# Kernel tuning notes

Hardware: AMD Instinct MI355X
Metric: run time of the kernel (lower is better)

Reference implementation:

```python
import jax, jax.numpy as jnp
import numpy as np

LN_EPS = 1e-5

def _conv2d(x, w, b, pad):
    # x: [B,C,H,W], w: [O,I,kh,kw] -> [B,O,H,W]
    y = jax.lax.conv_general_dilated(
        x, w, window_strides=(1, 1), padding=[(pad, pad), (pad, pad)],
        dimension_numbers=('NCHW', 'OIHW', 'NCHW'))
    return y + b[None, :, None, None]

def setup_inputs() -> dict:
    key = jax.random.key(0)
    ks = jax.random.split(key, 12)
    B, C, H, W = 4, 256, 64, 64
    D = 64  # inner_projection
    s_in = 1.0 / np.sqrt(C)
    s_d1 = 1.0 / np.sqrt(D)
    s_d3 = 1.0 / np.sqrt(D * 9)
    return {
        'x':     jax.random.normal(ks[0], (B, C, H, W), jnp.float32),
        'w_in':  jax.random.normal(ks[1], (D, C, 1, 1), jnp.float32) * s_in,
        'b_in':  jnp.zeros((D,), jnp.float32),
        'wq':    jax.random.normal(ks[2], (D, D, 3, 3), jnp.float32) * s_d3,
        'bq':    jnp.zeros((D,), jnp.float32),
        'wk':    jax.random.normal(ks[3], (D, D, 3, 3), jnp.float32) * s_d3,
        'bk':    jnp.zeros((D,), jnp.float32),
        'wv':    jax.random.normal(ks[4], (D, D, 3, 3), jnp.float32) * s_d3,
        'bv':    jnp.zeros((D,), jnp.float32),
        'w_out': jax.random.normal(ks[5], (C, D, 1, 1), jnp.float32) * s_d1,
        'b_out': jnp.zeros((C,), jnp.float32),
        'gamma': jax.random.normal(ks[6], (1,), jnp.float32) * 0.1,
        'ln_w':  jnp.ones((C,), jnp.float32),
        'ln_b':  jnp.zeros((C,), jnp.float32),
    }

def _attention(q, k, v):
    # full-pixel attention, NO 1/sqrt(d) scale (matches source)
    B, C, H, W = v.shape
    N = H * W
    qf = q.reshape(B, -1, N)   # [B,d,N]
    kf = k.reshape(B, -1, N)
    vf = v.reshape(B, -1, N)
    energy = jnp.einsum('bci,bcj->bij', qf, kf)      # [B,N,N] = Q^T K
    attn = jax.nn.softmax(energy, axis=-1)
    out = jnp.einsum('bcj,bij->bci', vf, attn)        # V @ attn^T
    return out.reshape(B, C, H, W)

def _layernorm2d(x, w, b):
    # normalize over channel dim per pixel (LayerNorm2d)
    mu = jnp.mean(x, axis=1, keepdims=True)
    var = jnp.var(x, axis=1, keepdims=True)
    xn = (x - mu) * jax.lax.rsqrt(var + LN_EPS)
    return xn * w[None, :, None, None] + b[None, :, None, None]

def reference(x, w_in, b_in, wq, bq, wk, bk, wv, bv, w_out, b_out, gamma, ln_w, ln_b):
    att = _conv2d(x, w_in, b_in, 0)          # inner projection [B,D,H,W]
    q = _conv2d(att, wq, bq, 1)
    k = _conv2d(att, wk, bk, 1)
    v = _conv2d(att, wv, bv, 1)
    att = _attention(q, k, v)
    att = _conv2d(att, w_out, b_out, 0)       # outer projection [B,C,H,W]
    return _layernorm2d(gamma * x + att, ln_w, ln_b)
```

## Files before the change

kernel.cpp:

```cpp
#include <hip/hip_runtime.h>
#include <hip/hip_bf16.h>

#define BB 4
#define CC 256
#define DD 64
#define HH 64
#define WW 64
#define NN 4096
#define NSPLIT 8
#define SM_SHIFT2 92.332482616893664f
#define LOG2E 1.4426950408889634f

typedef __hip_bfloat16 bf16;
typedef __attribute__((ext_vector_type(8))) short bf16x8;
typedef __attribute__((ext_vector_type(4))) float f32x4;
typedef __attribute__((ext_vector_type(4))) short s16x4;

#define MFMA16(a, b, c) __builtin_amdgcn_mfma_f32_16x16x32_bf16(a, b, c, 0, 0, 0)

#if __has_builtin(__builtin_amdgcn_mfma_f32_16x16x16bf16_1k)
static __device__ __forceinline__ f32x4 MFMA16K(s16x4 a, s16x4 b, f32x4 c) {
  return __builtin_amdgcn_mfma_f32_16x16x16bf16_1k(a, b, c, 0, 0, 0);
}
#else
static __device__ __forceinline__ f32x4 MFMA16K(s16x4 a, s16x4 b, f32x4 c) {
  f32x4 d;
  asm("v_mfma_f32_16x16x16_bf16 %0, %1, %2, %3"
      : "=&v"(d) : "v"(a), "v"(b), "v"(c));
  return d;
}
#endif

#if __has_builtin(__builtin_amdgcn_exp2f)
#define EXP2F(x) __builtin_amdgcn_exp2f(x)
#else
#define EXP2F(x) exp2f(x)
#endif

static __device__ __forceinline__ float ldin(const void* p, size_t i, bool isb) {
  return isb ? __bfloat162float(((const bf16*)p)[i]) : ((const float*)p)[i];
}
static __device__ __forceinline__ void stout(void* p, size_t i, float v, bool isb) {
  if (isb) ((bf16*)p)[i] = __float2bfloat16(v);
  else     ((float*)p)[i] = v;
}
static __device__ __forceinline__ unsigned pack2(bf16 a, bf16 b) {
  unsigned short ua = *reinterpret_cast<unsigned short*>(&a);
  unsigned short ub = *reinterpret_cast<unsigned short*>(&b);
  return (unsigned)ua | ((unsigned)ub << 16);
}
static __device__ __forceinline__ bool probe_bf16(const unsigned* lnw) {
  return lnw[0] == 0x3F803F80u;
}

__global__ __launch_bounds__(256) void k_wt(
    const void* __restrict__ wq, const void* __restrict__ wk,
    const void* __restrict__ wv, const void* __restrict__ w_in,
    const void* __restrict__ w_out,
    bf16* __restrict__ Wth, bf16* __restrict__ Wtl,
    bf16* __restrict__ Win_h, bf16* __restrict__ Win_l,
    bf16* __restrict__ Wo_h, bf16* __restrict__ Wo_l,
    const unsigned* __restrict__ lnw) {
  const bool isb = probe_bf16(lnw);
  int u = blockIdx.x * 256 + threadIdx.x;
  if (u < 110592) {
    int c3 = u / 36864, rem = u % 36864;
    int tap = rem / 4096, r2 = rem % 4096;
    int oc = r2 >> 6, ic = r2 & 63;
    const void* w = (c3 == 0) ? wq : ((c3 == 1) ? wk : wv);
    float v = ldin(w, (size_t)oc * 576 + ic * 9 + tap, isb);
    bf16 h = __float2bfloat16(v);
    Wth[u] = h;
    Wtl[u] = __float2bfloat16(v - __bfloat162float(h));
  } else if (u < 126976) {
    int v2 = u - 110592;
    float v = ldin(w_in, v2, isb);
    bf16 h = __float2bfloat16(v);
    Win_h[v2] = h;
    Win_l[v2] = __float2bfloat16(v - __bfloat162float(h));
  } else {
    int v2 = u - 126976;
    float v = ldin(w_out, v2, isb);
    bf16 h = __float2bfloat16(v);
    Wo_h[v2] = h;
    Wo_l[v2] = __float2bfloat16(v - __bfloat162float(h));
  }
}

__global__ __launch_bounds__(256) void k_conv_in(
    const void* __restrict__ x,
    const bf16* __restrict__ Win_h, const bf16* __restrict__ Win_l,
    const void* __restrict__ bias, bf16* __restrict__ att_h,
    bf16* __restrict__ att_l, const unsigned* __restrict__ lnw) {
  __shared__ __align__(16) short Xh[32 * 64];
  __shared__ __align__(16) short Xl[32 * 64];
  const bool isb = probe_bf16(lnw);
  const int b = blockIdx.y, n0 = blockIdx.x * 32;
  const int t = threadIdx.x;
  const int w = t >> 6, lane = t & 63, quad = lane >> 4, l16 = lane & 15;
  const int l7 = l16 & 7;
  const size_t xoff = (size_t)b * CC * NN;
  f32x4 acc[2];
  #pragma unroll
  for (int nt = 0; nt < 2; ++nt)
    #pragma unroll
    for (int r = 0; r < 4; ++r)
      acc[nt][r] = ldin(bias, w * 16 + quad * 4 + r, isb);
  for (int c0 = 0; c0 < CC; c0 += 64) {
    __syncthreads();
    #pragma unroll
    for (int i = 0; i < 4; ++i) {
      int u = t + i * 256;
      int dd = u >> 5, n = u & 31;
      float v0 = ldin(x, xoff + (size_t)(c0 + 2 * dd) * NN + n0 + n, isb);
      float v1 = ldin(x, xoff + (size_t)(c0 + 2 * dd + 1) * NN + n0 + n, isb);
      bf16 h0 = __float2bfloat16(v0), h1 = __float2bfloat16(v1);
      bf16 l0 = __float2bfloat16(v0 - __bfloat162float(h0));
      bf16 l1 = __float2bfloat16(v1 - __bfloat162float(h1));
      int cs = ((dd >> 2) ^ (n & 7)) * 8 + ((2 * dd) & 7);
      *(unsigned*)&Xh[n * 64 + cs] = pack2(h0, h1);
      *(unsigned*)&Xl[n * 64 + cs] = pack2(l0, l1);
    }
    __syncthreads();
    #pragma unroll
    for (int kc = 0; kc < 2; ++kc) {
      size_t woff = (size_t)(w * 16 + l16) * 256 + c0 + kc * 32 + quad * 8;
      bf16x8 wh = *(const bf16x8*)(Win_h + woff);
      bf16x8 wl = *(const bf16x8*)(Win_l + woff);
      const int xo = ((kc * 4 + quad) ^ l7) * 8;
      #pragma unroll
      for (int nt = 0; nt < 2; ++nt) {
        int rn = nt * 16 + l16;
        bf16x8 xh = *(const bf16x8*)&Xh[rn * 64 + xo];
        bf16x8 xl = *(const bf16x8*)&Xl[rn * 64 + xo];
        acc[nt] = MFMA16(wh, xh, acc[nt]);
        acc[nt] = MFMA16(wh, xl, acc[nt]);
        acc[nt] = MFMA16(wl, xh, acc[nt]);
      }
    }
  }
  #pragma unroll
  for (int nt = 0; nt < 2; ++nt) {
    size_t off = ((size_t)b * NN + n0 + nt * 16 + l16) * DD + w * 16 + quad * 4;
    bf16 h[4], l[4];
    #pragma unroll
    for (int r = 0; r < 4; ++r) {
      float v = acc[nt][r];
      h[r] = __float2bfloat16(v);
      l[r] = __float2bfloat16(v - __bfloat162float(h[r]));
    }
    *(uint2*)&att_h[off] = make_uint2(pack2(h[0], h[1]), pack2(h[2], h[3]));
    *(uint2*)&att_l[off] = make_uint2(pack2(l[0], l[1]), pack2(l[2], l[3]));
  }
}

__global__ __launch_bounds__(256) void k_conv3(
    const bf16* __restrict__ att_h, const bf16* __restrict__ att_l,
    const bf16* __restrict__ Wth, const bf16* __restrict__ Wtl,
    const void* __restrict__ bq, const void* __restrict__ bk,
    const void* __restrict__ bv,
    bf16* __restrict__ qth, bf16* __restrict__ qtl,
    bf16* __restrict__ kth, bf16* __restrict__ ktl,
    bf16* __restrict__ vt, const unsigned* __restrict__ lnw) {
  __shared__ __align__(16) short Ah[3 * 66 * 64];
  __shared__ __align__(16) short Al[3 * 66 * 64];
  float* o_s = reinterpret_cast<float*>(Ah);
  const bool isb = probe_bf16(lnw);
  const int y = blockIdx.x, b = blockIdx.y, c3 = blockIdx.z;
  const int t = threadIdx.x;
  const int w = t >> 6, lane = t & 63, quad = lane >> 4, l16 = lane & 15;
  const uint4 z4 = make_uint4(0, 0, 0, 0);
  #pragma unroll
  for (int r = 0; r < 3; ++r) {
    int yp = y + r - 1;
    bool ok = (unsigned)yp < 64u;
    const uint4* sh = (const uint4*)(att_h + ((size_t)b * NN + (size_t)yp * 64) * DD);
    const uint4* sl = (const uint4*)(att_l + ((size_t)b * NN + (size_t)yp * 64) * DD);
    #pragma unroll
    for (int ii = 0; ii < 2; ++ii) {
      int u = t + ii * 256;
      int xx = u >> 3, ch = u & 7;
      int rr = r * 66 + xx + 1;
      uint4 vh = ok ? sh[u] : z4;
      uint4 vl = ok ? sl[u] : z4;
      int cs = (ch ^ (rr & 7)) * 8;
      *(uint4*)&Ah[rr * 64 + cs] = vh;
      *(uint4*)&Al[rr * 64 + cs] = vl;
    }
    if (t < 16) {
      int rr = r * 66 + ((t & 1) ? 65 : 0);
      int cs = (t >> 1) * 8;
      *(uint4*)&Ah[rr * 64 + cs] = z4;
      *(uint4*)&Al[rr * 64 + cs] = z4;
    }
  }
  __syncthreads();
  const void* bp = (c3 == 0) ? bq : ((c3 == 1) ? bk : bv);
  const bf16* wth = Wth + (size_t)c3 * 9 * 4096;
  const bf16* wtl = Wtl + (size_t)c3 * 9 * 4096;
  f32x4 acc[4];
  #pragma unroll
  for (int nt = 0; nt < 4; ++nt)
    #pragma unroll
    for (int r = 0; r < 4; ++r)
      acc[nt][r] = ldin(bp, w * 16 + quad * 4 + r, isb);
  #pragma unroll
  for (int tap = 0; tap < 9; ++tap) {
    const int dy = tap / 3, dx = tap % 3;
    const int woff = tap * 4096 + (w * 16 + l16) * 64 + quad * 8;
    bf16x8 wh0 = *(const bf16x8*)(wth + woff);
    bf16x8 wh1 = *(const bf16x8*)(wth + woff + 32);
    bf16x8 wl0 = *(const bf16x8*)(wtl + woff);
    bf16x8 wl1 = *(const bf16x8*)(wtl + woff + 32);
    #pragma unroll
    for (int nt = 0; nt < 4; ++nt) {
      int rr = dy * 66 + nt * 16 + l16 + dx;
      int chA = (quad ^ (rr & 7)) * 8;
      int chB = ((quad + 4) ^ (rr & 7)) * 8;
      bf16x8 ah0 = *(const bf16x8*)&Ah[rr * 64 + chA];
      bf16x8 ah1 = *(const bf16x8*)&Ah[rr * 64 + chB];
      bf16x8 al0 = *(const bf16x8*)&Al[rr * 64 + chA];
      bf16x8 al1 = *(const bf16x8*)&Al[rr * 64 + chB];
      acc[nt] = MFMA16(wh0, ah0, acc[nt]);
      acc[nt] = MFMA16(wh1, ah1, acc[nt]);
      acc[nt] = MFMA16(wh0, al0, acc[nt]);
      acc[nt] = MFMA16(wh1, al1, acc[nt]);
      acc[nt] = MFMA16(wl0, ah0, acc[nt]);
      acc[nt] = MFMA16(wl1, ah1, acc[nt]);
    }
  }
  if (c3 < 2) {
    bf16* dh = (c3 == 0) ? qth : kth;
    bf16* dl = (c3 == 0) ? qtl : ktl;
    const float qsc = (c3 == 0) ? LOG2E : 1.0f;
    const size_t rowb = (size_t)b * NN + (size_t)y * 64;
    #pragma unroll
    for (int nt = 0; nt < 4; ++nt) {
      size_t off = (rowb + nt * 16 + l16) * DD + w * 16 + quad * 4;
      bf16 h[4], l[4];
      #pragma unroll
      for (int r = 0; r < 4; ++r) {
        float v = acc[nt][r] * qsc;
        h[r] = __float2bfloat16(v);
        l[r] = __float2bfloat16(v - __bfloat162float(h[r]));
      }
      *(uint2*)&dh[off] = make_uint2(pack2(h[0], h[1]), pack2(h[2], h[3]));
      *(uint2*)&dl[off] = make_uint2(pack2(l[0], l[1]), pack2(l[2], l[3]));
    }
  } else {
    __syncthreads();
    #pragma unroll
    for (int nt = 0; nt < 4; ++nt)
      #pragma unroll
      for (int r = 0; r < 4; ++r)
        o_s[(nt * 16 + l16) * 65 + w * 16 + quad * 4 + r] = acc[nt][r];
    __syncthreads();
    #pragma unroll
    for (int i = 0; i < 8; ++i) {
      int u = t + i * 256;
      int c = u >> 5, np = (u & 31) * 2;
      float v0 = o_s[np * 65 + c], v1 = o_s[(np + 1) * 65 + c];
      *(unsigned*)&vt[((size_t)b * DD + c) * NN + (size_t)y * 64 + np] =
          pack2(__float2bfloat16(v0), __float2bfloat16(v1));
    }
  }
}

__global__ __launch_bounds__(256) void k_attn(
    const bf16* __restrict__ qth, const bf16* __restrict__ qtl,
    const bf16* __restrict__ kth, const bf16* __restrict__ ktl,
    const bf16* __restrict__ vt, float* __restrict__ po,
    float* __restrict__ pl) {
  __shared__ __align__(16) short Kh[64 * 64];
  __shared__ __align__(16) short Kl[64 * 64];
  __shared__ __align__(16) short Vs[64 * 64];
  const int b = blockIdx.y, i0 = blockIdx.x * 128, sp = blockIdx.z;
  const int jt0 = sp * (64 / NSPLIT), jt1 = jt0 + (64 / NSPLIT);
  const int t = threadIdx.x;
  const int w = t >> 6, lane = t & 63, quad = lane >> 4, l16 = lane & 15;
  const int l7 = l16 & 7;
  const int xA = (quad ^ l7) * 8;
  const int xB = ((quad + 4) ^ l7) * 8;
  const int sr = t >> 2, m4 = t & 3, sg = m4 * 16;
  const int sc0 = ((2 * m4) ^ (sr & 7)) * 8;
  const int sc1 = ((2 * m4 + 1) ^ (sr & 7)) * 8;
  bf16x8 qf_h0[2], qf_h1[2], qf_l0[2], qf_l1[2];
  #pragma unroll
  for (int is = 0; is < 2; ++is) {
    size_t qoff = ((size_t)b * NN + i0 + is * 64 + w * 16 + l16) * DD + quad * 8;
    qf_h0[is] = *(const bf16x8*)(qth + qoff);
    qf_h1[is] = *(const bf16x8*)(qth + qoff + 32);
    qf_l0[is] = *(const bf16x8*)(qtl + qoff);
    qf_l1[is] = *(const bf16x8*)(qtl + qoff + 32);
  }
  uint4 kh0, kh1, kl0, kl1, vx0, vx1;
  {
    size_t koff = ((size_t)b * NN + jt0 * 64 + sr) * DD + sg;
    kh0 = ((const uint4*)(kth + koff))[0]; kh1 = ((const uint4*)(kth + koff))[1];
    kl0 = ((const uint4*)(ktl + koff))[0]; kl1 = ((const uint4*)(ktl + koff))[1];
    size_t voff = ((size_t)b * DD + sr) * NN + jt0 * 64 + sg;
    vx0 = ((const uint4*)(vt + voff))[0];  vx1 = ((const uint4*)(vt + voff))[1];
  }
  float l_run[2] = {0.f, 0.f};
  f32x4 oacc[4][2] = {};
  for (int jt = jt0; jt < jt1; ++jt) {
    __syncthreads();
    *(uint4*)&Kh[sr * 64 + sc0] = kh0;    *(uint4*)&Kh[sr * 64 + sc1] = kh1;
    *(uint4*)&Kl[sr * 64 + sc0] = kl0;    *(uint4*)&Kl[sr * 64 + sc1] = kl1;
    *(uint4*)&Vs[sr * 64 + sc0] = vx0;    *(uint4*)&Vs[sr * 64 + sc1] = vx1;
    __syncthreads();
    if (jt < jt1 - 1) {
      int j0n = (jt + 1) * 64;
      size_t koff = ((size_t)b * NN + j0n + sr) * DD + sg;
      kh0 = ((const uint4*)(kth + koff))[0]; kh1 = ((const uint4*)(kth + koff))[1];
      kl0 = ((const uint4*)(ktl + koff))[0]; kl1 = ((const uint4*)(ktl + koff))[1];
      size_t voff = ((size_t)b * DD + sr) * NN + j0n + sg;
      vx0 = ((const uint4*)(vt + voff))[0];  vx1 = ((const uint4*)(vt + voff))[1];
    }
    s16x4 pf[2][4];
    float psum[2] = {0.f, 0.f};
    #pragma unroll
    for (int mt = 0; mt < 4; ++mt) {
      int r0 = (mt * 16 + l16) * 64;
      bf16x8 kf_h0 = *(const bf16x8*)&Kh[r0 + xA];
      bf16x8 kf_h1 = *(const bf16x8*)&Kh[r0 + xB];
      bf16x8 kf_l0 = *(const bf16x8*)&Kl[r0 + xA];
      bf16x8 kf_l1 = *(const bf16x8*)&Kl[r0 + xB];
      #pragma unroll
      for (int is = 0; is < 2; ++is) {
        f32x4 c = {0.f, 0.f, 0.f, 0.f};
        c = MFMA16(kf_h0, qf_h0[is], c);
        c = MFMA16(kf_h1, qf_h1[is], c);
        c = MFMA16(kf_h0, qf_l0[is], c);
        c = MFMA16(kf_h1, qf_l1[is], c);
        c = MFMA16(kf_l0, qf_h0[is], c);
        c = MFMA16(kf_l1, qf_h1[is], c);
        s16x4 pk;
        float ps = 0.f;
        #pragma unroll
        for (int r = 0; r < 4; ++r) {
          float p = EXP2F(c[r] - SM_SHIFT2);
          bf16 ph = __float2bfloat16(p);
          ps += __bfloat162float(ph);
          pk[r] = *reinterpret_cast<short*>(&ph);
        }
        psum[is] += ps;
        pf[is][mt] = pk;
      }
    }
    #pragma unroll
    for (int is = 0; is < 2; ++is) {
      float ps = psum[is];
      ps += __shfl_xor(ps, 16, 64);
      ps += __shfl_xor(ps, 32, 64);
      l_run[is] += ps;
    }
    #pragma unroll
    for (int mt = 0; mt < 4; ++mt) {
      int rv = (mt * 16 + l16) * 64;
      #pragma unroll
      for (int kt = 0; kt < 4; ++kt) {
        s16x4 vf = *(const s16x4*)
            &Vs[rv + ((kt * 2 + (quad >> 1)) ^ l7) * 8 + (quad & 1) * 4];
        oacc[mt][0] = MFMA16K(vf, pf[0][kt], oacc[mt][0]);
        oacc[mt][1] = MFMA16K(vf, pf[1][kt], oacc[mt][1]);
      }
    }
  }
  const size_t SEGC = (size_t)BB * DD * NN;
  #pragma unroll
  for (int is = 0; is < 2; ++is) {
    const int ig = i0 + is * 64 + w * 16 + l16;
    #pragma unroll
    for (int mt = 0; mt < 4; ++mt)
      #pragma unroll
      for (int r = 0; r < 4; ++r) {
        int c = mt * 16 + quad * 4 + r;
        po[(size_t)sp * SEGC + ((size_t)b * DD + c) * NN + ig] = oacc[mt][is][r];
      }
    if (quad == 0) pl[((size_t)sp * BB + b) * NN + ig] = l_run[is];
  }
}

__global__ __launch_bounds__(256) void k_out_ln(
    const float* __restrict__ po, const float* __restrict__ pl,
    const void* __restrict__ x,
    const bf16* __restrict__ Wo_h, const bf16* __restrict__ Wo_l,
    const void* __restrict__ bias, const void* __restrict__ gamma,
    const void* __restrict__ lw, const void* __restrict__ lb,
    void* __restrict__ out, const unsigned* __restrict__ lnw) {
  __shared__ __align__(16) short Ahs[32 * 64];
  __shared__ __align__(16) short Als[32 * 64];
  __shared__ float inv_s[32];
  __shared__ float red1[32 * 4], red2[32 * 4];
  __shared__ float mu_s[32], rs_s[32];
  __shared__ float lw_s[256], lb_s[256];
  const bool isb = probe_bf16(lnw);
  const int b = blockIdx.y, n0 = blockIdx.x * 32;
  const int t = threadIdx.x;
  const int w = t >> 6, lane = t & 63, quad = lane >> 4, l16 = lane & 15;
  const int l7 = l16 & 7;
  const size_t SEGC = (size_t)BB * DD * NN;
  if (t < 32) {
    int i = n0 + t;
    float lsum = 0.f;
    #pragma unroll
    for (int s = 0; s < NSPLIT; ++s) lsum += pl[((size_t)s * BB + b) * NN + i];
    inv_s[t] = 1.f / lsum;
  }
  lw_s[t] = ldin(lw, t, isb);
  lb_s[t] = ldin(lb, t, isb);
  const float g = ldin(gamma, 0, isb);
  __syncthreads();
  #pragma unroll
  for (int i = 0; i < 4; ++i) {
    int u = t + i * 256;
    int dd = u >> 5, n = u & 31;
    size_t base = ((size_t)b * DD + 2 * dd) * NN + n0 + n;
    float v0 = 0.f, v1 = 0.f;
    #pragma unroll
    for (int s = 0; s < NSPLIT; ++s) {
      v0 += po[(size_t)s * SEGC + base];
      v1 += po[(size_t)s * SEGC + base + NN];
    }
    float inv = inv_s[n];
    v0 *= inv; v1 *= inv;
    bf16 h0 = __float2bfloat16(v0), h1 = __float2bfloat16(v1);
    bf16 l0 = __float2bfloat16(v0 - __bfloat162float(h0));
    bf16 l1 = __float2bfloat16(v1 - __bfloat162float(h1));
    int cs = ((dd >> 2) ^ (n & 7)) * 8 + ((2 * dd) & 7);
    *(unsigned*)&Ahs[n * 64 + cs] = pack2(h0, h1);
    *(unsigned*)&Als[n * 64 + cs] = pack2(l0, l1);
  }
  f32x4 acc[4][2];
  #pragma unroll
  for (int oct = 0; oct < 4; ++oct)
    #pragma unroll
    for (int r = 0; r < 4; ++r) {
      float bo = ldin(bias, w * 64 + oct * 16 + quad * 4 + r, isb);
      #pragma unroll
      for (int nt = 0; nt < 2; ++nt) acc[oct][nt][r] = bo;
    }
  __syncthreads();
  #pragma unroll
  for (int oct = 0; oct < 4; ++oct) {
    const int base = w * 64 + oct * 16;
    #pragma unroll
    for (int kc = 0; kc < 2; ++kc) {
      size_t woff = (size_t)(base + l16) * 64 + kc * 32 + quad * 8;
      bf16x8 wh = *(const bf16x8*)(Wo_h + woff);
      bf16x8 wl = *(const bf16x8*)(Wo_l + woff);
      const int xo = ((kc * 4 + quad) ^ l7) * 8;
      #pragma unroll
      for (int nt = 0; nt < 2; ++nt) {
        int rn = nt * 16 + l16;
        bf16x8 ah = *(const bf16x8*)&Ahs[rn * 64 + xo];
        bf16x8 al = *(const bf16x8*)&Als[rn * 64 + xo];
        acc[oct][nt] = MFMA16(wh, ah, acc[oct][nt]);
        acc[oct][nt] = MFMA16(wh, al, acc[oct][nt]);
        acc[oct][nt] = MFMA16(wl, ah, acc[oct][nt]);
      }
    }
  }
  #pragma unroll
  for (int nt = 0; nt < 2; ++nt) {
    int nn = nt * 16 + l16;
    float s1 = 0.f, s2 = 0.f;
    #pragma unroll
    for (int oct = 0; oct < 4; ++oct)
      #pragma unroll
      for (int r = 0; r < 4; ++r) {
        int oc = w * 64 + oct * 16 + quad * 4 + r;
        float xv = ldin(x, ((size_t)b * CC + oc) * NN + n0 + nn, isb);
        float y = acc[oct][nt][r] + g * xv;
        acc[oct][nt][r] = y;
        s1 += y; s2 += y * y;
      }
    s1 += __shfl_xor(s1, 16, 64); s1 += __shfl_xor(s1, 32, 64);
    s2 += __shfl_xor(s2, 16, 64); s2 += __shfl_xor(s2, 32, 64);
    if (quad == 0) { red1[nn * 4 + w] = s1; red2[nn * 4 + w] = s2; }
  }
  __syncthreads();
  if (t < 32) {
    float sm = red1[t * 4] + red1[t * 4 + 1] + red1[t * 4 + 2] + red1[t * 4 + 3];
    float sq = red2[t * 4] + red2[t * 4 + 1] + red2[t * 4 + 2] + red2[t * 4 + 3];
    float mu = sm * (1.f / 256.f);
    float var = sq * (1.f / 256.f) - mu * mu;
    mu_s[t] = mu;
    rs_s[t] = rsqrtf(var + 1e-5f);
  }
  __syncthreads();
  #pragma unroll
  for (int nt = 0; nt < 2; ++nt) {
    int nn = nt * 16 + l16;
    float mu = mu_s[nn], rs = rs_s[nn];
    #pragma unroll
    for (int oct = 0; oct < 4; ++oct)
      #pragma unroll
      for (int r = 0; r < 4; ++r) {
        int oc = w * 64 + oct * 16 + quad * 4 + r;
        float o = (acc[oct][nt][r] - mu) * rs * lw_s[oc] + lb_s[oc];
        stout(out, ((size_t)b * CC + oc) * NN + n0 + nn, o, isb);
      }
  }
}

extern "C" void kernel_launch(void* const* d_in, const int* in_sizes, int n_in,
                              void* d_out, int out_size, void* d_ws, size_t ws_size,
                              hipStream_t stream) {
  const void* x     = d_in[0];
  const void* w_in  = d_in[1];
  const void* b_in  = d_in[2];
  const void* wq    = d_in[3];
  const void* bq    = d_in[4];
  const void* wk    = d_in[5];
  const void* bk    = d_in[6];
  const void* wv    = d_in[7];
  const void* bv    = d_in[8];
  const void* w_out = d_in[9];
  const void* b_out = d_in[10];
  const void* gamma = d_in[11];
  const void* ln_w  = d_in[12];
  const void* ln_b  = d_in[13];

  const size_t SEG = (size_t)BB * DD * NN;
  char*  p     = (char*)d_ws;
  bf16*  att_h = (bf16*)p;  p += SEG * 2;
  bf16*  att_l = (bf16*)p;  p += SEG * 2;
  bf16*  qth   = (bf16*)p;  p += SEG * 2;
  bf16*  qtl   = (bf16*)p;  p += SEG * 2;
  bf16*  kth   = (bf16*)p;  p += SEG * 2;
  bf16*  ktl   = (bf16*)p;  p += SEG * 2;
  bf16*  vt    = (bf16*)p;  p += SEG * 2;
  float* po    = (float*)p; p += (size_t)NSPLIT * SEG * 4;
  float* pl    = (float*)p; p += (size_t)NSPLIT * BB * NN * 4;
  bf16*  Wth   = (bf16*)p;  p += 110592 * 2;
  bf16*  Wtl   = (bf16*)p;  p += 110592 * 2;
  bf16*  Win_h = (bf16*)p;  p += 16384 * 2;
  bf16*  Win_l = (bf16*)p;  p += 16384 * 2;
  bf16*  Wo_h  = (bf16*)p;  p += 16384 * 2;
  bf16*  Wo_l  = (bf16*)p;  p += 16384 * 2;
  const unsigned* lnw = (const unsigned*)ln_w;

  k_wt<<<560, 256, 0, stream>>>(wq, wk, wv, w_in, w_out, Wth, Wtl,
                                Win_h, Win_l, Wo_h, Wo_l, lnw);
  k_conv_in<<<dim3(NN / 32, BB), 256, 0, stream>>>(x, Win_h, Win_l, b_in,
                                                   att_h, att_l, lnw);
  k_conv3<<<dim3(64, BB, 3), 256, 0, stream>>>(att_h, att_l, Wth, Wtl,
                                               bq, bk, bv,
                                               qth, qtl, kth, ktl, vt, lnw);
  k_attn<<<dim3(NN / 128, BB, NSPLIT), 256, 0, stream>>>(qth, qtl, kth, ktl, vt,
                                                         po, pl);
  k_out_ln<<<dim3(NN / 32, BB), 256, 0, stream>>>(po, pl, x, Wo_h, Wo_l,
                                                  b_out, gamma, ln_w, ln_b,
                                                  d_out, lnw);
}
```

Measured before the change: 177.2 us.

## Double-buffer attention K/V tiles, halve split count, fuse conv3 q/k/v into one block

The attention kernel now double-buffers the K/V tiles in shared memory, cutting one barrier per iteration so the next tile's stores overlap compute. It also raises wave priority around the MFMA sections. The split count over keys drops from 8 to 4, which reduces partial-output traffic and reduction work in the output kernel but also halves the number of attention blocks. The 3x3 conv kernel now loops over q, k and v inside one block instead of launching three grid slices, so the staged input rows are reused, at the cost of fewer blocks running in parallel.

```diff
diff --git a/kernel.cpp b/kernel.cpp
--- a/kernel.cpp
+++ b/kernel.cpp
@@ -7,7 +7,7 @@
 #define HH 64
 #define WW 64
 #define NN 4096
-#define NSPLIT 8
+#define NSPLIT 4
 #define SM_SHIFT2 92.332482616893664f
 #define LOG2E 1.4426950408889634f
 
@@ -166,7 +166,7 @@
   __shared__ __align__(16) short Al[3 * 66 * 64];
   float* o_s = reinterpret_cast<float*>(Ah);
   const bool isb = probe_bf16(lnw);
-  const int y = blockIdx.x, b = blockIdx.y, c3 = blockIdx.z;
+  const int y = blockIdx.x, b = blockIdx.y;
   const int t = threadIdx.x;
   const int w = t >> 6, lane = t & 63, quad = lane >> 4, l16 = lane & 15;
   const uint4 z4 = make_uint4(0, 0, 0, 0);
@@ -195,73 +195,76 @@
     }
   }
   __syncthreads();
-  const void* bp = (c3 == 0) ? bq : ((c3 == 1) ? bk : bv);
-  const bf16* wth = Wth + (size_t)c3 * 9 * 4096;
-  const bf16* wtl = Wtl + (size_t)c3 * 9 * 4096;
-  f32x4 acc[4];
-  #pragma unroll
-  for (int nt = 0; nt < 4; ++nt)
-    #pragma unroll
-    for (int r = 0; r < 4; ++r)
-      acc[nt][r] = ldin(bp, w * 16 + quad * 4 + r, isb);
-  #pragma unroll
-  for (int tap = 0; tap < 9; ++tap) {
-    const int dy = tap / 3, dx = tap % 3;
-    const int woff = tap * 4096 + (w * 16 + l16) * 64 + quad * 8;
-    bf16x8 wh0 = *(const bf16x8*)(wth + woff);
-    bf16x8 wh1 = *(const bf16x8*)(wth + woff + 32);
-    bf16x8 wl0 = *(const bf16x8*)(wtl + woff);
-    bf16x8 wl1 = *(const bf16x8*)(wtl + woff + 32);
-    #pragma unroll
-    for (int nt = 0; nt < 4; ++nt) {
-      int rr = dy * 66 + nt * 16 + l16 + dx;
-      int chA = (quad ^ (rr & 7)) * 8;
-      int chB = ((quad + 4) ^ (rr & 7)) * 8;
-      bf16x8 ah0 = *(const bf16x8*)&Ah[rr * 64 + chA];
-      bf16x8 ah1 = *(const bf16x8*)&Ah[rr * 64 + chB];
-      bf16x8 al0 = *(const bf16x8*)&Al[rr * 64 + chA];
-      bf16x8 al1 = *(const bf16x8*)&Al[rr * 64 + chB];
-      acc[nt] = MFMA16(wh0, ah0, acc[nt]);
-      acc[nt] = MFMA16(wh1, ah1, acc[nt]);
-      acc[nt] = MFMA16(wh0, al0, acc[nt]);
-      acc[nt] = MFMA16(wh1, al1, acc[nt]);
-      acc[nt] = MFMA16(wl0, ah0, acc[nt]);
-      acc[nt] = MFMA16(wl1, ah1, acc[nt]);
-    }
-  }
-  if (c3 < 2) {
-    bf16* dh = (c3 == 0) ? qth : kth;
-    bf16* dl = (c3 == 0) ? qtl : ktl;
-    const float qsc = (c3 == 0) ? LOG2E : 1.0f;
-    const size_t rowb = (size_t)b * NN + (size_t)y * 64;
-    #pragma unroll
-    for (int nt = 0; nt < 4; ++nt) {
-      size_t off = (rowb + nt * 16 + l16) * DD + w * 16 + quad * 4;
-      bf16 h[4], l[4];
-      #pragma unroll
-      for (int r = 0; r < 4; ++r) {
-        float v = acc[nt][r] * qsc;
-        h[r] = __float2bfloat16(v);
-        l[r] = __float2bfloat16(v - __bfloat162float(h[r]));
-      }
-      *(uint2*)&dh[off] = make_uint2(pack2(h[0], h[1]), pack2(h[2], h[3]));
-      *(uint2*)&dl[off] = make_uint2(pack2(l[0], l[1]), pack2(l[2], l[3]));
-    }
-  } else {
-    __syncthreads();
+  #pragma unroll 1
+  for (int c3 = 0; c3 < 3; ++c3) {
+    const void* bp = (c3 == 0) ? bq : ((c3 == 1) ? bk : bv);
+    const bf16* wth = Wth + (size_t)c3 * 9 * 4096;
+    const bf16* wtl = Wtl + (size_t)c3 * 9 * 4096;
+    f32x4 acc[4];
     #pragma unroll
     for (int nt = 0; nt < 4; ++nt)
       #pragma unroll
       for (int r = 0; r < 4; ++r)
-        o_s[(nt * 16 + l16) * 65 + w * 16 + quad * 4 + r] = acc[nt][r];
-    __syncthreads();
-    #pragma unroll
-    for (int i = 0; i < 8; ++i) {
-      int u = t + i * 256;
-      int c = u >> 5, np = (u & 31) * 2;
-      float v0 = o_s[np * 65 + c], v1 = o_s[(np + 1) * 65 + c];
-      *(unsigned*)&vt[((size_t)b * DD + c) * NN + (size_t)y * 64 + np] =
-          pack2(__float2bfloat16(v0), __float2bfloat16(v1));
+        acc[nt][r] = ldin(bp, w * 16 + quad * 4 + r, isb);
+    #pragma unroll
+    for (int tap = 0; tap < 9; ++tap) {
+      const int dy = tap / 3, dx = tap % 3;
+      const int woff = tap * 4096 + (w * 16 + l16) * 64 + quad * 8;
+      bf16x8 wh0 = *(const bf16x8*)(wth + woff);
+      bf16x8 wh1 = *(const bf16x8*)(wth + woff + 32);
+      bf16x8 wl0 = *(const bf16x8*)(wtl + woff);
+      bf16x8 wl1 = *(const bf16x8*)(wtl + woff + 32);
+      #pragma unroll
+      for (int nt = 0; nt < 4; ++nt) {
+        int rr = dy * 66 + nt * 16 + l16 + dx;
+        int chA = (quad ^ (rr & 7)) * 8;
+        int chB = ((quad + 4) ^ (rr & 7)) * 8;
+        bf16x8 ah0 = *(const bf16x8*)&Ah[rr * 64 + chA];
+        bf16x8 ah1 = *(const bf16x8*)&Ah[rr * 64 + chB];
+        bf16x8 al0 = *(const bf16x8*)&Al[rr * 64 + chA];
+        bf16x8 al1 = *(const bf16x8*)&Al[rr * 64 + chB];
+        acc[nt] = MFMA16(wh0, ah0, acc[nt]);
+        acc[nt] = MFMA16(wh1, ah1, acc[nt]);
+        acc[nt] = MFMA16(wh0, al0, acc[nt]);
+        acc[nt] = MFMA16(wh1, al1, acc[nt]);
+        acc[nt] = MFMA16(wl0, ah0, acc[nt]);
+        acc[nt] = MFMA16(wl1, ah1, acc[nt]);
+      }
+    }
+    if (c3 < 2) {
+      bf16* dh = (c3 == 0) ? qth : kth;
+      bf16* dl = (c3 == 0) ? qtl : ktl;
+      const float qsc = (c3 == 0) ? LOG2E : 1.0f;
+      const size_t rowb = (size_t)b * NN + (size_t)y * 64;
+      #pragma unroll
+      for (int nt = 0; nt < 4; ++nt) {
+        size_t off = (rowb + nt * 16 + l16) * DD + w * 16 + quad * 4;
+        bf16 h[4], l[4];
+        #pragma unroll
+        for (int r = 0; r < 4; ++r) {
+          float v = acc[nt][r] * qsc;
+          h[r] = __float2bfloat16(v);
+          l[r] = __float2bfloat16(v - __bfloat162float(h[r]));
+        }
+        *(uint2*)&dh[off] = make_uint2(pack2(h[0], h[1]), pack2(h[2], h[3]));
+        *(uint2*)&dl[off] = make_uint2(pack2(l[0], l[1]), pack2(l[2], l[3]));
+      }
+    } else {
+      __syncthreads();
+      #pragma unroll
+      for (int nt = 0; nt < 4; ++nt)
+        #pragma unroll
+        for (int r = 0; r < 4; ++r)
+          o_s[(nt * 16 + l16) * 65 + w * 16 + quad * 4 + r] = acc[nt][r];
+      __syncthreads();
+      #pragma unroll
+      for (int i = 0; i < 8; ++i) {
+        int u = t + i * 256;
+        int c = u >> 5, np = (u & 31) * 2;
+        float v0 = o_s[np * 65 + c], v1 = o_s[(np + 1) * 65 + c];
+        *(unsigned*)&vt[((size_t)b * DD + c) * NN + (size_t)y * 64 + np] =
+            pack2(__float2bfloat16(v0), __float2bfloat16(v1));
+      }
     }
   }
 }
@@ -271,9 +274,9 @@
     const bf16* __restrict__ kth, const bf16* __restrict__ ktl,
     const bf16* __restrict__ vt, float* __restrict__ po,
     float* __restrict__ pl) {
-  __shared__ __align__(16) short Kh[64 * 64];
-  __shared__ __align__(16) short Kl[64 * 64];
-  __shared__ __align__(16) short Vs[64 * 64];
+  __shared__ __align__(16) short Kh[2][64 * 64];
+  __shared__ __align__(16) short Kl[2][64 * 64];
+  __shared__ __align__(16) short Vs[2][64 * 64];
   const int b = blockIdx.y, i0 = blockIdx.x * 128, sp = blockIdx.z;
   const int jt0 = sp * (64 / NSPLIT), jt1 = jt0 + (64 / NSPLIT);
   const int t = threadIdx.x;
@@ -301,14 +304,14 @@
     size_t voff = ((size_t)b * DD + sr) * NN + jt0 * 64 + sg;
     vx0 = ((const uint4*)(vt + voff))[0];  vx1 = ((const uint4*)(vt + voff))[1];
   }
+  *(uint4*)&Kh[0][sr * 64 + sc0] = kh0;  *(uint4*)&Kh[0][sr * 64 + sc1] = kh1;
+  *(uint4*)&Kl[0][sr * 64 + sc0] = kl0;  *(uint4*)&Kl[0][sr * 64 + sc1] = kl1;
+  *(uint4*)&Vs[0][sr * 64 + sc0] = vx0;  *(uint4*)&Vs[0][sr * 64 + sc1] = vx1;
+  __syncthreads();
   float l_run[2] = {0.f, 0.f};
   f32x4 oacc[4][2] = {};
+  int p = 0;
   for (int jt = jt0; jt < jt1; ++jt) {
-    __syncthreads();
-    *(uint4*)&Kh[sr * 64 + sc0] = kh0;    *(uint4*)&Kh[sr * 64 + sc1] = kh1;
-    *(uint4*)&Kl[sr * 64 + sc0] = kl0;    *(uint4*)&Kl[sr * 64 + sc1] = kl1;
-    *(uint4*)&Vs[sr * 64 + sc0] = vx0;    *(uint4*)&Vs[sr * 64 + sc1] = vx1;
-    __syncthreads();
     if (jt < jt1 - 1) {
       int j0n = (jt + 1) * 64;
       size_t koff = ((size_t)b * NN + j0n + sr) * DD + sg;
@@ -317,15 +320,19 @@
       size_t voff = ((size_t)b * DD + sr) * NN + j0n + sg;
       vx0 = ((const uint4*)(vt + voff))[0];  vx1 = ((const uint4*)(vt + voff))[1];
     }
+    const short* khp = Kh[p];
+    const short* klp = Kl[p];
+    const short* vsp = Vs[p];
     s16x4 pf[2][4];
     float psum[2] = {0.f, 0.f};
     #pragma unroll
     for (int mt = 0; mt < 4; ++mt) {
       int r0 = (mt * 16 + l16) * 64;
-      bf16x8 kf_h0 = *(const bf16x8*)&Kh[r0 + xA];
-      bf16x8 kf_h1 = *(const bf16x8*)&Kh[r0 + xB];
-      bf16x8 kf_l0 = *(const bf16x8*)&Kl[r0 + xA];
-      bf16x8 kf_l1 = *(const bf16x8*)&Kl[r0 + xB];
+      bf16x8 kf_h0 = *(const bf16x8*)&khp[r0 + xA];
+      bf16x8 kf_h1 = *(const bf16x8*)&khp[r0 + xB];
+      bf16x8 kf_l0 = *(const bf16x8*)&klp[r0 + xA];
+      bf16x8 kf_l1 = *(const bf16x8*)&klp[r0 + xB];
+      __builtin_amdgcn_s_setprio(1);
       #pragma unroll
       for (int is = 0; is < 2; ++is) {
         f32x4 c = {0.f, 0.f, 0.f, 0.f};
@@ -339,14 +346,15 @@
         float ps = 0.f;
         #pragma unroll
         for (int r = 0; r < 4; ++r) {
-          float p = EXP2F(c[r] - SM_SHIFT2);
-          bf16 ph = __float2bfloat16(p);
+          float pexp = EXP2F(c[r] - SM_SHIFT2);
+          bf16 ph = __float2bfloat16(pexp);
           ps += __bfloat162float(ph);
           pk[r] = *reinterpret_cast<short*>(&ph);
         }
         psum[is] += ps;
         pf[is][mt] = pk;
       }
+      __builtin_amdgcn_s_setprio(0);
     }
     #pragma unroll
     for (int is = 0; is < 2; ++is) {
@@ -355,17 +363,29 @@
       ps += __shfl_xor(ps, 32, 64);
       l_run[is] += ps;
     }
+    __builtin_amdgcn_s_setprio(1);
     #pragma unroll
     for (int mt = 0; mt < 4; ++mt) {
       int rv = (mt * 16 + l16) * 64;
       #pragma unroll
       for (int kt = 0; kt < 4; ++kt) {
         s16x4 vf = *(const s16x4*)
-            &Vs[rv + ((kt * 2 + (quad >> 1)) ^ l7) * 8 + (quad & 1) * 4];
+            &vsp[rv + ((kt * 2 + (quad >> 1)) ^ l7) * 8 + (quad & 1) * 4];
         oacc[mt][0] = MFMA16K(vf, pf[0][kt], oacc[mt][0]);
         oacc[mt][1] = MFMA16K(vf, pf[1][kt], oacc[mt][1]);
       }
     }
+    __builtin_amdgcn_s_setprio(0);
+    if (jt < jt1 - 1) {
+      short* khn = Kh[p ^ 1];
+      short* kln = Kl[p ^ 1];
+      short* vsn = Vs[p ^ 1];
+      *(uint4*)&khn[sr * 64 + sc0] = kh0;  *(uint4*)&khn[sr * 64 + sc1] = kh1;
+      *(uint4*)&kln[sr * 64 + sc0] = kl0;  *(uint4*)&kln[sr * 64 + sc1] = kl1;
+      *(uint4*)&vsn[sr * 64 + sc0] = vx0;  *(uint4*)&vsn[sr * 64 + sc1] = vx1;
+    }
+    __syncthreads();
+    p ^= 1;
   }
   const size_t SEGC = (size_t)BB * DD * NN;
   #pragma unroll
@@ -546,9 +566,9 @@
                                 Win_h, Win_l, Wo_h, Wo_l, lnw);
   k_conv_in<<<dim3(NN / 32, BB), 256, 0, stream>>>(x, Win_h, Win_l, b_in,
                                                    att_h, att_l, lnw);
-  k_conv3<<<dim3(64, BB, 3), 256, 0, stream>>>(att_h, att_l, Wth, Wtl,
-                                               bq, bk, bv,
-                                               qth, qtl, kth, ktl, vt, lnw);
+  k_conv3<<<dim3(64, BB), 256, 0, stream>>>(att_h, att_l, Wth, Wtl,
+                                            bq, bk, bv,
+                                            qth, qtl, kth, ktl, vt, lnw);
   k_attn<<<dim3(NN / 128, BB, NSPLIT), 256, 0, stream>>>(qth, qtl, kth, ktl, vt,
                                                          po, pl);
   k_out_ln<<<dim3(NN / 32, BB), 256, 0, stream>>>(po, pl, x, Wo_h, Wo_l,
```

Result: slower. 184.0 us (+3.9%).
